# Kernel optimization log

Measured on AMD Instinct MI355X. Metric: run time of the kernel, lower is better.

## Reference

```python
import jax, jax.numpy as jnp
import numpy as np

N_NODES = 50000
N_EDGES = 1_600_000
IN_F = 128
OUT_F = 32
HEADS = 4
EDGE_F = 4
EDGE_HID = 32


def setup_inputs() -> dict:
    key = jax.random.key(0)
    ks = jax.random.split(key, 12)
    x = jax.random.normal(ks[0], (N_NODES, IN_F), dtype=jnp.float32)
    edge_index = jax.random.randint(ks[1], (2, N_EDGES), 0, N_NODES, dtype=jnp.int32)
    edge_attr = jax.random.normal(ks[2], (N_EDGES, EDGE_F), dtype=jnp.float32)
    # linear: in_features -> heads*out_features (stored as [in, out] for x @ W)
    W = jax.random.normal(ks[3], (IN_F, HEADS * OUT_F), dtype=jnp.float32) * (1.0 / np.sqrt(IN_F))
    b = jnp.zeros((HEADS * OUT_F,), dtype=jnp.float32)
    # edge_proj: Linear(EDGE_F,32) -> ReLU -> Linear(32, heads)
    eW1 = jax.random.normal(ks[4], (EDGE_F, EDGE_HID), dtype=jnp.float32) * (1.0 / np.sqrt(EDGE_F))
    eb1 = jnp.zeros((EDGE_HID,), dtype=jnp.float32)
    eW2 = jax.random.normal(ks[5], (EDGE_HID, HEADS), dtype=jnp.float32) * (1.0 / np.sqrt(EDGE_HID))
    eb2 = jnp.zeros((HEADS,), dtype=jnp.float32)
    att_src = jax.random.normal(ks[6], (1, HEADS, OUT_F), dtype=jnp.float32) * 0.1
    att_dst = jax.random.normal(ks[7], (1, HEADS, OUT_F), dtype=jnp.float32) * 0.1
    return {"x": x, "edge_index": edge_index, "edge_attr": edge_attr,
            "W": W, "b": b, "eW1": eW1, "eb1": eb1, "eW2": eW2, "eb2": eb2,
            "att_src": att_src, "att_dst": att_dst}


def reference(x, edge_index, edge_attr, W, b, eW1, eb1, eW2, eb2, att_src, att_dst):
    N = x.shape[0]
    src, dst = edge_index[0], edge_index[1]
    E = src.shape[0]

    h = (x @ W + b).reshape(N, HEADS, OUT_F)                     # [N,H,F]
    alpha_src = jnp.sum(h[src] * att_src, axis=-1)               # [E,H]
    alpha_dst = jnp.sum(h[dst] * att_dst, axis=-1)               # [E,H]
    edge_att = jax.nn.relu(edge_attr @ eW1 + eb1) @ eW2 + eb2    # [E,H]
    alpha = jax.nn.leaky_relu(alpha_src + alpha_dst + edge_att, negative_slope=0.2)

    # softmax_by_src: dense [N,H] buffer of -inf, scatter-set by src
    # softmax over the NODE axis, then gather back per edge.
    last = jax.ops.segment_max(jnp.arange(E, dtype=jnp.int32), src, num_segments=N)  # [N]
    valid = last >= 0
    dense = jnp.where(valid[:, None], alpha[jnp.clip(last, 0)], -jnp.inf)  # [N,H]
    dense = jax.nn.softmax(dense, axis=0)
    alpha_e = dense[src]                                         # [E,H]

    # dropout: module default training=False path (identity), eval mode
    # scatter-add aggregation: out[src] += h[dst] * alpha_e (all heads at once)
    msg = h[dst] * alpha_e[:, :, None]                           # [E,H,F]
    out = jnp.zeros_like(h).at[src].add(msg)                     # [N,H,F]
    return out.mean(axis=1)                                      # [N,F]
```

## Files before the change

kernel.cpp:

```cpp
#include <hip/hip_runtime.h>
#include <hip/hip_fp16.h>
#include <math.h>


#define SUPCAP 9216
#define AGG_CAP 2048
#define BIN_CHUNK 2048

__global__ __launch_bounds__(256, 3) void k_pre(
    const float* __restrict__ x, const float* __restrict__ W,
    const float* __restrict__ b, const float* __restrict__ att_src,
    const float* __restrict__ att_dst, __half* __restrict__ hbuf16,
    float* __restrict__ s_, float* __restrict__ t_,
    const int* __restrict__ src, const int* __restrict__ dst,
    int* __restrict__ bcur, uint2* __restrict__ bin2,
    int N, int E, int nsup, int ngemm, int nbin) {
  __shared__ __align__(16) float smem[12672];
  int tx = threadIdx.x;
  int bid = blockIdx.x;
  int mmin = (nbin < ngemm) ? nbin : ngemm;
  int m2 = 2 * mmin;
  bool isbin;
  int wid;
  if (bid < m2) { isbin = (bid & 1); wid = bid >> 1; }
  else { isbin = (nbin > ngemm); wid = mmin + (bid - m2); }

  if (isbin) {
    uint2* ebuf = (uint2*)smem;
    int* hist = (int*)(smem + 4096);
    int* bas  = hist + 256;
    int* curs = bas + 256;
    int* gpos = curs + 256;
    int e0 = wid * BIN_CHUNK;
    int n = E - e0; if (n > BIN_CHUNK) n = BIN_CHUNK;
    hist[tx] = 0;
    __syncthreads();
    for (int i = tx; i < n; i += 256) {
      atomicAdd(&hist[src[e0 + i] >> 8], 1);
    }
    __syncthreads();
    int v = hist[tx];
    bas[tx] = v;
    __syncthreads();
    for (int off = 1; off < 256; off <<= 1) {
      int t = (tx >= off) ? bas[tx - off] : 0;
      __syncthreads();
      bas[tx] += t;
      __syncthreads();
    }
    curs[tx] = bas[tx] - v;
    if (tx < nsup && v > 0) gpos[tx] = atomicAdd(&bcur[tx], v);
    __syncthreads();
    for (int i = tx; i < n; i += 256) {
      int e = e0 + i;
      int s = src[e], d = dst[e];
      int pos = atomicAdd(&curs[s >> 8], 1);
      unsigned loc = (unsigned)(s & 255);
      ebuf[pos] = make_uint2((loc << 24) | (unsigned)e, (loc << 16) | (unsigned)d);
    }
    __syncthreads();
    for (int i = tx; i < n; i += 256) {
      uint2 w = ebuf[i];
      int lo = 0, hi = 255;
      while (lo < hi) {
        int mid = (lo + hi) >> 1;
        if (bas[mid] > i) hi = mid; else lo = mid + 1;
      }
      int bb = lo;
      int lbase = bas[bb] - hist[bb];
      int off = gpos[bb] + (i - lbase);
      if (off < SUPCAP) {
        bin2[(size_t)bb * SUPCAP + off] = w;
      }
    }
  } else {
    float* xs = smem;
    float* ws = smem + 64 * 132;
    int r0 = wid * 64;
    const float4* xg = (const float4*)(x + (size_t)r0 * 128);
#pragma unroll
    for (int j = 0; j < 8; ++j) {
      int l = tx + j * 256;
      int row = l >> 5, col4 = l & 31;
      float4 v = make_float4(0.f, 0.f, 0.f, 0.f);
      if (r0 + row < N) v = xg[l];
      *(float4*)(xs + row * 132 + col4 * 4) = v;
    }
    int cg = tx & 15, rg = tx >> 4;
    float acc[4][8];
#pragma unroll
    for (int r = 0; r < 4; ++r)
#pragma unroll
      for (int c = 0; c < 8; ++c) acc[r][c] = 0.f;
    const float4* Wg4 = (const float4*)W;
    const float* xbase = xs + rg * 4 * 132;
    int woff = cg * 8 + ((cg >> 3) << 2);
    for (int kt = 0; kt < 4; ++kt) {
      __syncthreads();
#pragma unroll
      for (int j = 0; j < 4; ++j) {
        int ll = tx + j * 256;
        int row = ll >> 5, c4 = ll & 31;
        *(float4*)(ws + row * 132 + c4 * 4 + ((c4 >> 4) << 2)) = Wg4[kt * 1024 + ll];
      }
      __syncthreads();
#pragma unroll 2
      for (int k4 = 0; k4 < 8; ++k4) {
        float4 xr0 = *(const float4*)(xbase + kt * 32 + k4 * 4);
        float4 xr1 = *(const float4*)(xbase + 132 + kt * 32 + k4 * 4);
        float4 xr2 = *(const float4*)(xbase + 264 + kt * 32 + k4 * 4);
        float4 xr3 = *(const float4*)(xbase + 396 + kt * 32 + k4 * 4);
#pragma unroll
        for (int kk = 0; kk < 4; ++kk) {
          const float* wrow = ws + (k4 * 4 + kk) * 132 + woff;
          float4 w0 = *(const float4*)(wrow);
          float4 w1 = *(const float4*)(wrow + 4);
          const float wc[8] = {w0.x, w0.y, w0.z, w0.w, w1.x, w1.y, w1.z, w1.w};
          float xv0 = ((const float*)&xr0)[kk];
          float xv1 = ((const float*)&xr1)[kk];
          float xv2 = ((const float*)&xr2)[kk];
          float xv3 = ((const float*)&xr3)[kk];
#pragma unroll
          for (int c = 0; c < 8; ++c) {
            acc[0][c] += xv0 * wc[c];
            acc[1][c] += xv1 * wc[c];
            acc[2][c] += xv2 * wc[c];
            acc[3][c] += xv3 * wc[c];
          }
        }
      }
    }
    float4 b0 = ((const float4*)b)[cg * 2],       b1 = ((const float4*)b)[cg * 2 + 1];
    float4 s0 = ((const float4*)att_src)[cg * 2], s1 = ((const float4*)att_src)[cg * 2 + 1];
    float4 d0 = ((const float4*)att_dst)[cg * 2], d1 = ((const float4*)att_dst)[cg * 2 + 1];
    const float bbv[8] = {b0.x, b0.y, b0.z, b0.w, b1.x, b1.y, b1.z, b1.w};
    const float asv[8] = {s0.x, s0.y, s0.z, s0.w, s1.x, s1.y, s1.z, s1.w};
    const float adv[8] = {d0.x, d0.y, d0.z, d0.w, d1.x, d1.y, d1.z, d1.w};
    int hd = cg >> 2;
#pragma unroll
    for (int r = 0; r < 4; ++r) {
      float o[8];
#pragma unroll
      for (int c = 0; c < 8; ++c) o[c] = acc[r][c] + bbv[c];
      float sp = 0.f, tp = 0.f;
#pragma unroll
      for (int c = 0; c < 8; ++c) { sp += o[c] * asv[c]; tp += o[c] * adv[c]; }
      sp += __shfl_xor(sp, 1); sp += __shfl_xor(sp, 2);
      tp += __shfl_xor(tp, 1); tp += __shfl_xor(tp, 2);
      int grow = r0 + rg * 4 + r;
      if (grow < N) {
        __half2 h0 = __floats2half2_rn(o[0], o[1]);
        __half2 h1 = __floats2half2_rn(o[2], o[3]);
        __half2 h2 = __floats2half2_rn(o[4], o[5]);
        __half2 h3 = __floats2half2_rn(o[6], o[7]);
        uint4 u;
        u.x = *(unsigned*)&h0; u.y = *(unsigned*)&h1;
        u.z = *(unsigned*)&h2; u.w = *(unsigned*)&h3;
        ((uint4*)(hbuf16 + (size_t)grow * 128))[cg] = u;
        if ((tx & 3) == 0) {
          s_[grow * 4 + hd] = sp;
          t_[grow * 4 + hd] = tp;
        }
      }
    }
  }
}

__global__ __launch_bounds__(1024, 1) void k_dense(
    const int* __restrict__ bcur, const uint2* __restrict__ bin2,
    const int* __restrict__ dst, const float* __restrict__ edge_attr,
    const float* __restrict__ eW1, const float* __restrict__ eb1,
    const float* __restrict__ eW2, const float* __restrict__ eb2,
    const float* __restrict__ s_, const float* __restrict__ t_,
    float* __restrict__ dense, float* __restrict__ pmax,
    float* __restrict__ psum,
    unsigned short* __restrict__ sorted_dst,
    int* __restrict__ noff, int* __restrict__ ncnt, int N) {
  __shared__ int lastv[256];
  __shared__ int hist[256], bas[256], curs[256];
  __shared__ float lm[256 * 4], ls[256 * 4];
  int sp = blockIdx.x, tx = threadIdx.x;
  if (tx < 256) { lastv[tx] = -1; hist[tx] = 0; }
  __syncthreads();
  int cnt = bcur[sp]; if (cnt > SUPCAP) cnt = SUPCAP;
  const uint2* b2 = bin2 + (size_t)sp * SUPCAP;
  for (int i = tx; i < cnt; i += 1024) {
    uint2 w = b2[i];
    atomicMax(&lastv[w.x >> 24], (int)(w.x & 0xFFFFFF));
    atomicAdd(&hist[w.y >> 16], 1);
  }
  __syncthreads();
  int v = 0;
  if (tx < 256) { v = hist[tx]; bas[tx] = v; }
  __syncthreads();
  for (int off = 1; off < 256; off <<= 1) {
    int t = 0;
    if (tx < 256 && tx >= off) t = bas[tx - off];
    __syncthreads();
    if (tx < 256) bas[tx] += t;
    __syncthreads();
  }
  int gn = sp * 256 + tx;
  if (tx < 256) {
    curs[tx] = bas[tx] - v;
    noff[gn] = sp * SUPCAP + bas[tx] - v;
    ncnt[gn] = v;
  }
  __syncthreads();
  unsigned short* sd = sorted_dst + (size_t)sp * SUPCAP;
  for (int i = tx; i < cnt; i += 1024) {
    unsigned y = b2[i].y;
    int pos = atomicAdd(&curs[y >> 16], 1);
    sd[pos] = (unsigned short)y;
  }
  float vv[4] = {-INFINITY, -INFINITY, -INFINITY, -INFINITY};
  if (tx < 256 && gn < N) {
    int e = lastv[tx];
    if (e >= 0) {
      int d = dst[e];
      const float* ea = edge_attr + (size_t)e * 4;
      float e0 = ea[0], e1 = ea[1], e2 = ea[2], e3 = ea[3];
      float a0 = eb2[0], a1 = eb2[1], a2 = eb2[2], a3 = eb2[3];
#pragma unroll
      for (int i = 0; i < 32; ++i) {
        float hid = eb1[i] + e0 * eW1[i] + e1 * eW1[32 + i] + e2 * eW1[64 + i] + e3 * eW1[96 + i];
        hid = fmaxf(hid, 0.f);
        a0 += hid * eW2[i * 4 + 0]; a1 += hid * eW2[i * 4 + 1];
        a2 += hid * eW2[i * 4 + 2]; a3 += hid * eW2[i * 4 + 3];
      }
      float w0 = s_[gn * 4 + 0] + t_[d * 4 + 0] + a0;
      float w1 = s_[gn * 4 + 1] + t_[d * 4 + 1] + a1;
      float w2 = s_[gn * 4 + 2] + t_[d * 4 + 2] + a2;
      float w3 = s_[gn * 4 + 3] + t_[d * 4 + 3] + a3;
      vv[0] = w0 > 0.f ? w0 : 0.2f * w0;
      vv[1] = w1 > 0.f ? w1 : 0.2f * w1;
      vv[2] = w2 > 0.f ? w2 : 0.2f * w2;
      vv[3] = w3 > 0.f ? w3 : 0.2f * w3;
    }
#pragma unroll
    for (int h = 0; h < 4; ++h) dense[gn * 4 + h] = vv[h];
  }
  if (tx < 256) {
#pragma unroll
    for (int h = 0; h < 4; ++h) {
      lm[tx * 4 + h] = vv[h];
      ls[tx * 4 + h] = (vv[h] > -INFINITY) ? 1.f : 0.f;
    }
  }
  __syncthreads();
  for (int off = 128; off > 0; off >>= 1) {
    if (tx < off) {
#pragma unroll
      for (int h = 0; h < 4; ++h) {
        float m2 = lm[(tx + off) * 4 + h], s2 = ls[(tx + off) * 4 + h];
        float m1 = lm[tx * 4 + h], s1 = ls[tx * 4 + h];
        float M = fmaxf(m1, m2);
        if (M > -INFINITY) {
          ls[tx * 4 + h] = s1 * expf(m1 - M) + s2 * expf(m2 - M);
          lm[tx * 4 + h] = M;
        }
      }
    }
    __syncthreads();
  }
  if (tx == 0) {
#pragma unroll
    for (int h = 0; h < 4; ++h) {
      pmax[sp * 4 + h] = lm[h];
      psum[sp * 4 + h] = ls[h];
    }
  }
}

#define ACC(r, P, Q) { \
  float2 f0 = __half22float2(*(__half2*)&r.x), f1 = __half22float2(*(__half2*)&r.y); \
  float2 f2 = __half22float2(*(__half2*)&r.z), f3 = __half22float2(*(__half2*)&r.w); \
  P.x += f0.x; P.y += f0.y; P.z += f1.x; P.w += f1.y; \
  Q.x += f2.x; Q.y += f2.y; Q.z += f3.x; Q.w += f3.y; }

__global__ __launch_bounds__(256) void k_agg(
    const unsigned short* __restrict__ sorted_dst,
    const int* __restrict__ noff, const int* __restrict__ ncnt,
    const __half* __restrict__ hbuf16, const float* __restrict__ dense,
    const float* __restrict__ pmax, const float* __restrict__ psum, int nb,
    float* __restrict__ out, int N) {
  __shared__ unsigned short sl[AGG_CAP];
  __shared__ float lm[256], ls[256];
  __shared__ float sgm[4], sgi[4];
  int tx = threadIdx.x;
  int n0 = blockIdx.x << 4;
  int nlast = n0 + 15; if (nlast > N - 1) nlast = N - 1;
  int lstart = noff[n0];
  int lend = noff[nlast] + ncnt[nlast];
  int total = lend - lstart; if (total > AGG_CAP) total = AGG_CAP;
  for (int i = tx; i < total; i += 256) sl[i] = sorted_dst[lstart + i];
  {
    int h = tx & 3, chunk = tx >> 2;
    float m = -INFINITY, s = 0.f;
    for (int bq = chunk; bq < nb; bq += 64) {
      float m2 = pmax[bq * 4 + h], s2 = psum[bq * 4 + h];
      float M = fmaxf(m, m2);
      if (M > -INFINITY) {
        s = s * expf(m - M) + s2 * expf(m2 - M);
        m = M;
      }
    }
    lm[tx] = m; ls[tx] = s;
    __syncthreads();
    for (int off = 128; off >= 4; off >>= 1) {
      if (tx < off) {
        float m2 = lm[tx + off], s2 = ls[tx + off];
        float m1 = lm[tx], s1 = ls[tx];
        float M = fmaxf(m1, m2);
        if (M > -INFINITY) {
          ls[tx] = s1 * expf(m1 - M) + s2 * expf(m2 - M);
          lm[tx] = M;
        }
      }
      __syncthreads();
    }
    if (tx < 4) {
      sgm[tx] = lm[tx];
      sgi[tx] = 1.f / ls[tx];
    }
    __syncthreads();
  }
  int g = tx >> 4, l = tx & 15;
  int n = n0 + g;
  if (n >= N) return;
  int beg = noff[n] - lstart;
  int cnt = ncnt[n];
  if (beg + cnt > total) cnt = total - beg;
  int end = beg + cnt;
  int hd = l >> 2;
  float w = expf(dense[(size_t)n * 4 + hd] - sgm[hd]) * sgi[hd];
  float4 p0 = {0, 0, 0, 0}, q0 = {0, 0, 0, 0};
  float4 p1 = {0, 0, 0, 0}, q1 = {0, 0, 0, 0};
  int e = beg;
  for (; e + 7 < end; e += 8) {
    int c0 = sl[e],     c1 = sl[e + 1], c2 = sl[e + 2], c3 = sl[e + 3];
    int c4_ = sl[e + 4], c5 = sl[e + 5], c6 = sl[e + 6], c7 = sl[e + 7];
    uint4 r0 = *((const uint4*)(hbuf16 + ((size_t)c0  << 7)) + l);
    uint4 r1 = *((const uint4*)(hbuf16 + ((size_t)c1  << 7)) + l);
    uint4 r2 = *((const uint4*)(hbuf16 + ((size_t)c2  << 7)) + l);
    uint4 r3 = *((const uint4*)(hbuf16 + ((size_t)c3  << 7)) + l);
    uint4 r4 = *((const uint4*)(hbuf16 + ((size_t)c4_ << 7)) + l);
    uint4 r5 = *((const uint4*)(hbuf16 + ((size_t)c5  << 7)) + l);
    uint4 r6 = *((const uint4*)(hbuf16 + ((size_t)c6  << 7)) + l);
    uint4 r7 = *((const uint4*)(hbuf16 + ((size_t)c7  << 7)) + l);
    ACC(r0, p0, q0); ACC(r1, p1, q1); ACC(r2, p0, q0); ACC(r3, p1, q1);
    ACC(r4, p0, q0); ACC(r5, p1, q1); ACC(r6, p0, q0); ACC(r7, p1, q1);
  }
  for (; e + 3 < end; e += 4) {
    int c0 = sl[e], c1 = sl[e + 1], c2 = sl[e + 2], c3 = sl[e + 3];
    uint4 r0 = *((const uint4*)(hbuf16 + ((size_t)c0 << 7)) + l);
    uint4 r1 = *((const uint4*)(hbuf16 + ((size_t)c1 << 7)) + l);
    uint4 r2 = *((const uint4*)(hbuf16 + ((size_t)c2 << 7)) + l);
    uint4 r3 = *((const uint4*)(hbuf16 + ((size_t)c3 << 7)) + l);
    ACC(r0, p0, q0); ACC(r1, p1, q1); ACC(r2, p0, q0); ACC(r3, p1, q1);
  }
  for (; e < end; ++e) {
    int c0 = sl[e];
    uint4 r0 = *((const uint4*)(hbuf16 + ((size_t)c0 << 7)) + l);
    ACC(r0, p0, q0);
  }
  p0.x += p1.x; p0.y += p1.y; p0.z += p1.z; p0.w += p1.w;
  q0.x += q1.x; q0.y += q1.y; q0.z += q1.z; q0.w += q1.w;
  p0.x *= w; p0.y *= w; p0.z *= w; p0.w *= w;
  q0.x *= w; q0.y *= w; q0.z *= w; q0.w *= w;
  p0.x += __shfl_xor(p0.x, 4);  p0.y += __shfl_xor(p0.y, 4);
  p0.z += __shfl_xor(p0.z, 4);  p0.w += __shfl_xor(p0.w, 4);
  q0.x += __shfl_xor(q0.x, 4);  q0.y += __shfl_xor(q0.y, 4);
  q0.z += __shfl_xor(q0.z, 4);  q0.w += __shfl_xor(q0.w, 4);
  p0.x += __shfl_xor(p0.x, 8);  p0.y += __shfl_xor(p0.y, 8);
  p0.z += __shfl_xor(p0.z, 8);  p0.w += __shfl_xor(p0.w, 8);
  q0.x += __shfl_xor(q0.x, 8);  q0.y += __shfl_xor(q0.y, 8);
  q0.z += __shfl_xor(q0.z, 8);  q0.w += __shfl_xor(q0.w, 8);
  if (l < 4) {
    float4 oA, oB;
    oA.x = 0.25f * p0.x; oA.y = 0.25f * p0.y; oA.z = 0.25f * p0.z; oA.w = 0.25f * p0.w;
    oB.x = 0.25f * q0.x; oB.y = 0.25f * q0.y; oB.z = 0.25f * q0.z; oB.w = 0.25f * q0.w;
    *(float4*)(out + (size_t)n * 32 + l * 8) = oA;
    *(float4*)(out + (size_t)n * 32 + l * 8 + 4) = oB;
  }
}

extern "C" void kernel_launch(void* const* d_in, const int* in_sizes, int n_in,
                              void* d_out, int out_size, void* d_ws, size_t ws_size,
                              hipStream_t stream) {
  const float* x        = (const float*)d_in[0];
  const int*   ei       = (const int*)d_in[1];
  const float* edge_attr= (const float*)d_in[2];
  const float* W        = (const float*)d_in[3];
  const float* b        = (const float*)d_in[4];
  const float* eW1      = (const float*)d_in[5];
  const float* eb1      = (const float*)d_in[6];
  const float* eW2      = (const float*)d_in[7];
  const float* eb2      = (const float*)d_in[8];
  const float* att_src  = (const float*)d_in[9];
  const float* att_dst  = (const float*)d_in[10];
  float* out = (float*)d_out;

  const int N = in_sizes[0] / 128;
  const int E = in_sizes[1] / 2;
  const int* src = ei;
  const int* dst = ei + E;
  const int NSUP = (N + 255) >> 8;

  char* wp = (char*)d_ws;
  auto alloc = [&](size_t bytes) -> void* {
    void* p = (void*)wp;
    wp += (bytes + 255) & ~(size_t)255;
    return p;
  };
  __half* hbuf16 = (__half*)alloc((size_t)N * 128 * 2);
  float* s_    = (float*)alloc((size_t)N * 4 * 4);
  float* t_    = (float*)alloc((size_t)N * 4 * 4);
  float* dense = (float*)alloc((size_t)N * 4 * 4);
  float* pmax  = (float*)alloc((size_t)NSUP * 4 * 4);
  float* psum  = (float*)alloc((size_t)NSUP * 4 * 4);
  int* bcur    = (int*)alloc((size_t)NSUP * 4);
  uint2* bin2  = (uint2*)alloc((size_t)NSUP * SUPCAP * 8);
  unsigned short* sorted_dst = (unsigned short*)alloc((size_t)NSUP * SUPCAP * 2);
  int* noff    = (int*)alloc((size_t)NSUP * 256 * 4);
  int* ncnt    = (int*)alloc((size_t)NSUP * 256 * 4);

  const int NGEMM = (N + 63) / 64;
  const int NBIN  = (E + BIN_CHUNK - 1) / BIN_CHUNK;

  hipMemsetAsync(bcur, 0, (size_t)NSUP * 4, stream);
  k_pre<<<NGEMM + NBIN, 256, 0, stream>>>(x, W, b, att_src, att_dst, hbuf16, s_, t_,
                                          src, dst, bcur, bin2,
                                          N, E, NSUP, NGEMM, NBIN);
  k_dense<<<NSUP, 1024, 0, stream>>>(bcur, bin2, dst, edge_attr, eW1, eb1, eW2, eb2,
                                     s_, t_, dense, pmax, psum, sorted_dst, noff, ncnt, N);
  k_agg<<<(N + 15) / 16, 256, 0, stream>>>(sorted_dst, noff, ncnt, hbuf16, dense,
                                           pmax, psum, NSUP, out, N);
}
```

Baseline: 224.4 us.

## Compute node projection GEMM in fp16 with fdot2 and halve LDS footprint

Converts the x and W tiles to half precision when staging them into shared memory, packing W as k-pairs so the inner loop can use v_dot2 fp16 instructions that accumulate into fp32. Shared memory per block shrinks, so the launch bound is raised from 3 to 4 blocks per CU for higher occupancy. The aim is to cut FMA count and LDS traffic in the projection GEMM. In exchange, x and W are rounded to fp16 before the multiply, which lowers input precision.

```diff
diff --git a/kernel.cpp b/kernel.cpp
--- a/kernel.cpp
+++ b/kernel.cpp
@@ -7,7 +7,12 @@
 #define AGG_CAP 2048
 #define BIN_CHUNK 2048
 
-__global__ __launch_bounds__(256, 3) void k_pre(
+typedef _Float16 half2_t __attribute__((ext_vector_type(2)));
+__device__ __forceinline__ half2_t h2cast(unsigned u) {
+  return __builtin_bit_cast(half2_t, u);
+}
+
+__global__ __launch_bounds__(256, 4) void k_pre(
     const float* __restrict__ x, const float* __restrict__ W,
     const float* __restrict__ b, const float* __restrict__ att_src,
     const float* __restrict__ att_dst, __half* __restrict__ hbuf16,
@@ -15,7 +20,7 @@
     const int* __restrict__ src, const int* __restrict__ dst,
     int* __restrict__ bcur, uint2* __restrict__ bin2,
     int N, int E, int nsup, int ngemm, int nbin) {
-  __shared__ __align__(16) float smem[12672];
+  __shared__ __align__(16) float smem[6656];
   int tx = threadIdx.x;
   int bid = blockIdx.x;
   int mmin = (nbin < ngemm) ? nbin : ngemm;
@@ -74,8 +79,8 @@
       }
     }
   } else {
-    float* xs = smem;
-    float* ws = smem + 64 * 132;
+    __half* xs = (__half*)smem;
+    char* wsb = (char*)smem + 17408;
     int r0 = wid * 64;
     const float4* xg = (const float4*)(x + (size_t)r0 * 128);
 #pragma unroll
@@ -84,7 +89,10 @@
       int row = l >> 5, col4 = l & 31;
       float4 v = make_float4(0.f, 0.f, 0.f, 0.f);
       if (r0 + row < N) v = xg[l];
-      *(float4*)(xs + row * 132 + col4 * 4) = v;
+      __half2 p0 = __floats2half2_rn(v.x, v.y);
+      __half2 p1 = __floats2half2_rn(v.z, v.w);
+      uint2 u; u.x = *(unsigned*)&p0; u.y = *(unsigned*)&p1;
+      *(uint2*)(xs + row * 136 + col4 * 4) = u;
     }
     int cg = tx & 15, rg = tx >> 4;
     float acc[4][8];
@@ -93,39 +101,54 @@
 #pragma unroll
       for (int c = 0; c < 8; ++c) acc[r][c] = 0.f;
     const float4* Wg4 = (const float4*)W;
-    const float* xbase = xs + rg * 4 * 132;
-    int woff = cg * 8 + ((cg >> 3) << 2);
+    const __half* xbase = xs + rg * 4 * 136;
+    int wcg = cg * 32 + ((cg >> 2) << 4);
     for (int kt = 0; kt < 4; ++kt) {
       __syncthreads();
 #pragma unroll
-      for (int j = 0; j < 4; ++j) {
-        int ll = tx + j * 256;
-        int row = ll >> 5, c4 = ll & 31;
-        *(float4*)(ws + row * 132 + c4 * 4 + ((c4 >> 4) << 2)) = Wg4[kt * 1024 + ll];
+      for (int j = 0; j < 2; ++j) {
+        int it = tx + j * 256;
+        int kp = it >> 5, c4 = it & 31;
+        float4 wa = Wg4[(kt * 32 + kp * 2) * 32 + c4];
+        float4 wb = Wg4[(kt * 32 + kp * 2 + 1) * 32 + c4];
+        __half2 q0 = __floats2half2_rn(wa.x, wb.x);
+        __half2 q1 = __floats2half2_rn(wa.y, wb.y);
+        __half2 q2 = __floats2half2_rn(wa.z, wb.z);
+        __half2 q3 = __floats2half2_rn(wa.w, wb.w);
+        uint4 u;
+        u.x = *(unsigned*)&q0; u.y = *(unsigned*)&q1;
+        u.z = *(unsigned*)&q2; u.w = *(unsigned*)&q3;
+        int cb = c4 >> 1;
+        int off = kp * 576 + cb * 32 + ((cb >> 2) << 4) + ((c4 & 1) << 4);
+        *(uint4*)(wsb + off) = u;
       }
       __syncthreads();
-#pragma unroll 2
-      for (int k4 = 0; k4 < 8; ++k4) {
-        float4 xr0 = *(const float4*)(xbase + kt * 32 + k4 * 4);
-        float4 xr1 = *(const float4*)(xbase + 132 + kt * 32 + k4 * 4);
-        float4 xr2 = *(const float4*)(xbase + 264 + kt * 32 + k4 * 4);
-        float4 xr3 = *(const float4*)(xbase + 396 + kt * 32 + k4 * 4);
-#pragma unroll
-        for (int kk = 0; kk < 4; ++kk) {
-          const float* wrow = ws + (k4 * 4 + kk) * 132 + woff;
-          float4 w0 = *(const float4*)(wrow);
-          float4 w1 = *(const float4*)(wrow + 4);
-          const float wc[8] = {w0.x, w0.y, w0.z, w0.w, w1.x, w1.y, w1.z, w1.w};
-          float xv0 = ((const float*)&xr0)[kk];
-          float xv1 = ((const float*)&xr1)[kk];
-          float xv2 = ((const float*)&xr2)[kk];
-          float xv3 = ((const float*)&xr3)[kk];
-#pragma unroll
-          for (int c = 0; c < 8; ++c) {
-            acc[0][c] += xv0 * wc[c];
-            acc[1][c] += xv1 * wc[c];
-            acc[2][c] += xv2 * wc[c];
-            acc[3][c] += xv3 * wc[c];
+#pragma unroll
+      for (int k8 = 0; k8 < 4; ++k8) {
+        uint4 xr[4];
+#pragma unroll
+        for (int rr = 0; rr < 4; ++rr)
+          xr[rr] = *(const uint4*)(xbase + rr * 136 + kt * 32 + k8 * 8);
+#pragma unroll
+        for (int kp = 0; kp < 4; ++kp) {
+          const char* wrow = wsb + (k8 * 4 + kp) * 576 + wcg;
+          uint4 wlo = *(const uint4*)(wrow);
+          uint4 whi = *(const uint4*)(wrow + 16);
+          half2_t wv0 = h2cast(wlo.x), wv1 = h2cast(wlo.y);
+          half2_t wv2 = h2cast(wlo.z), wv3 = h2cast(wlo.w);
+          half2_t wv4 = h2cast(whi.x), wv5 = h2cast(whi.y);
+          half2_t wv6 = h2cast(whi.z), wv7 = h2cast(whi.w);
+#pragma unroll
+          for (int rr = 0; rr < 4; ++rr) {
+            half2_t xp = h2cast(((const unsigned*)&xr[rr])[kp]);
+            acc[rr][0] = __builtin_amdgcn_fdot2(xp, wv0, acc[rr][0], false);
+            acc[rr][1] = __builtin_amdgcn_fdot2(xp, wv1, acc[rr][1], false);
+            acc[rr][2] = __builtin_amdgcn_fdot2(xp, wv2, acc[rr][2], false);
+            acc[rr][3] = __builtin_amdgcn_fdot2(xp, wv3, acc[rr][3], false);
+            acc[rr][4] = __builtin_amdgcn_fdot2(xp, wv4, acc[rr][4], false);
+            acc[rr][5] = __builtin_amdgcn_fdot2(xp, wv5, acc[rr][5], false);
+            acc[rr][6] = __builtin_amdgcn_fdot2(xp, wv6, acc[rr][6], false);
+            acc[rr][7] = __builtin_amdgcn_fdot2(xp, wv7, acc[rr][7], false);
           }
         }
       }
```

Result: faster. 214.4 us, median of 2 (-4.5%).
